# Performance work log

Measured on AMD Instinct MI355X. Metric: run time of the kernel, lower is better.

## Reference

```python
import jax, jax.numpy as jnp
import numpy as np

DIM = 512
HEADS = 8
DIM_HEAD = 64
VID = (8, 32, 32)   # (frames, height, width)
KS = (3, 3, 3)      # odd kernel sizes
DIL = (1, 1, 1)


def _build_indices():
    F, H, W = VID
    kf, kh, kw = KS
    df, dh, dw = DIL
    pf, ph, pw = df * (kf - 1) // 2, dh * (kh - 1) // 2, dw * (kw - 1) // 2
    Fp, Hp, Wp = F + 2 * pf, H + 2 * ph, W + 2 * pw
    N = F * H * W
    ff, yy, xx = np.meshgrid(np.arange(F), np.arange(H), np.arange(W), indexing='ij')
    of, oy, ox = np.meshgrid(np.arange(kf) * df, np.arange(kh) * dh, np.arange(kw) * dw, indexing='ij')
    nf = ff[..., None, None, None] + of   # (F,H,W,kf,kh,kw) coords in padded volume
    ny = yy[..., None, None, None] + oy
    nx = xx[..., None, None, None] + ox
    nbr = ((nf * Hp + ny) * Wp + nx).reshape(N, -1)  # (N, K) flat indices into padded volume
    sf, sy, sx = nf - pf, ny - ph, nx - pw           # source coords in unpadded volume
    valid = (sf >= 0) & (sf < F) & (sy >= 0) & (sy < H) & (sx >= 0) & (sx < W)
    tok = np.where(valid, (sf * H + sy) * W + sx, N).reshape(N, -1)  # sentinel N = padding
    mask = np.arange(N)[:, None] < tok               # causal mask; sentinel N always masked
    mask = np.concatenate([np.zeros((N, 1), bool), mask], axis=1)    # bos column never masked
    return jnp.asarray(nbr), jnp.asarray(mask), ((pf, pf), (ph, ph), (pw, pw))

_NBR, _MASK, _PAD = _build_indices()


def setup_inputs() -> dict:
    key = jax.random.key(0)
    ks = jax.random.split(key, 6)
    F, H, W = VID
    n = F * H * W + 1
    inner = HEADS * DIM_HEAD
    s = DIM ** -0.5
    return {
        "x":     jax.random.normal(ks[0], (1, n, DIM), jnp.float32),
        "w_q":   jax.random.normal(ks[1], (DIM, inner), jnp.float32) * s,
        "w_kv":  jax.random.normal(ks[2], (DIM, 2 * inner), jnp.float32) * s,
        "w_th":  jax.random.normal(ks[3], (HEADS, HEADS), jnp.float32) * HEADS ** -0.5,
        "w_out": jax.random.normal(ks[4], (inner, DIM), jnp.float32) * inner ** -0.5,
        "b_out": jnp.zeros((DIM,), jnp.float32),
    }


def reference(x, w_q, w_kv, w_th, w_out, b_out):
    b, n, _ = x.shape
    F, H, W = VID
    N = F * H * W  # n == N + 1 (BOS token first)
    h, d = HEADS, DIM_HEAD
    q = x @ w_q
    k, v = jnp.split(x @ w_kv, 2, axis=-1)

    def heads(t):
        return t.reshape(b, n, h, d).transpose(0, 2, 1, 3).reshape(b * h, n, d)

    q = heads(q) * d ** -0.5
    k, v = heads(k), heads(v)
    q = q[:, 1:]
    k_bos, k = k[:, :1], k[:, 1:]
    v_bos, v = v[:, :1], v[:, 1:]

    def unfold(t):  # gather 3D local neighborhoods: (bh, N, d) -> (bh, N, K, d)
        vol = jnp.pad(t.reshape(b * h, F, H, W, d), ((0, 0),) + _PAD + ((0, 0),))
        return vol.reshape(b * h, -1, d)[:, _NBR]

    kj = jnp.concatenate([jnp.broadcast_to(k_bos[:, None], (b * h, N, 1, d)), unfold(k)], axis=2)
    vj = jnp.concatenate([jnp.broadcast_to(v_bos[:, None], (b * h, N, 1, d)), unfold(v)], axis=2)

    sim = jnp.einsum('bid,bijd->bij', q, kj)                  # (bh, N, K+1)
    sim = jnp.where(_MASK[None], jnp.finfo(sim.dtype).min, sim)
    attn = jax.nn.softmax(sim, axis=-1)                       # stable_softmax == shift-invariant softmax
    attn = jnp.einsum('gh,bhij->bgij', w_th, attn.reshape(b, h, N, -1)).reshape(b * h, N, -1)
    out = jnp.einsum('bij,bijd->bid', attn, vj)               # (bh, N, d)
    out = jnp.concatenate([v_bos, out], axis=1)               # prepend bos value passthrough
    out = out.reshape(b, h, n, d).transpose(0, 2, 1, 3).reshape(b, n, h * d)
    return out @ w_out + b_out
```

## Files before the change

kernel.cpp:

```cpp
#include <hip/hip_runtime.h>
#include <stdint.h>

#define DIMC 512
#define INNER 512
#define NTOK 8192
#define NSEQ 8193
#define MPAD1 8448
#define QKV_COLS 1536

#define CONV_XT   (MPAD1 * DIMC / 4)
#define CONV_WQKV (QKV_COLS * DIMC)
#define CONV_WOUT (INNER * DIMC)
#define CONV_TOT  (CONV_XT + CONV_WQKV + CONV_WOUT)

typedef __attribute__((ext_vector_type(8))) short bf16x8;
typedef __attribute__((ext_vector_type(4))) float f32x4;
typedef __attribute__((ext_vector_type(8))) unsigned short u16x8;

__device__ __forceinline__ float bf2f(unsigned short u) {
  return __uint_as_float(((unsigned int)u) << 16);
}
__device__ __forceinline__ unsigned short f2bf(float f) {
  unsigned int x = __float_as_uint(f);
  unsigned int lsb = (x >> 16) & 1u;
  x += 0x7fffu + lsb;
  return (unsigned short)(x >> 16);
}

__device__ __forceinline__ void gload_lds16(const unsigned short* g, unsigned short* l) {
  __builtin_amdgcn_global_load_lds(
      (const __attribute__((address_space(1))) void*)g,
      (__attribute__((address_space(3))) void*)l, 16, 0, 0);
}

__global__ void k_conv(const float* __restrict__ x, const float* __restrict__ wq,
                       const float* __restrict__ wkv, const float* __restrict__ wout,
                       unsigned short* __restrict__ xb, unsigned short* __restrict__ wqkvT,
                       unsigned short* __restrict__ woutT) {
  const int gid = blockIdx.x * 256 + threadIdx.x;
  if (gid < CONV_XT) {
    const int idx = gid * 4;
    const int row = idx / DIMC;
    ushort4 o;
    if (row < NSEQ) {
      const float4 v = *(const float4*)(x + idx);
      o.x = f2bf(v.x); o.y = f2bf(v.y); o.z = f2bf(v.z); o.w = f2bf(v.w);
    } else {
      o.x = 0; o.y = 0; o.z = 0; o.w = 0;
    }
    *(ushort4*)(xb + idx) = o;
  } else if (gid < CONV_XT + CONV_WQKV) {
    const int idx = gid - CONV_XT;
    const int c = idx / DIMC, k = idx % DIMC;
    const float v = (c < INNER) ? wq[k * INNER + c] * 0.125f
                                : wkv[k * (2 * INNER) + (c - INNER)];
    wqkvT[idx] = f2bf(v);
  } else {
    const int idx = gid - CONV_XT - CONV_WQKV;
    const int c = idx / DIMC, k = idx % DIMC;
    woutT[idx] = f2bf(wout[k * DIMC + c]);
  }
}

template <int BM, int BN, int TN, int LDC, bool OUT_BF16>
__global__ __launch_bounds__((BM == 256) ? 512 : 256)
void k_gemm(const unsigned short* __restrict__ A,
            const unsigned short* __restrict__ BT,
            void* __restrict__ C,
            const float* __restrict__ bias,
            int Mreal) {
  constexpr int NW = (BM == 256) ? 8 : 4;
  constexpr int MF = (BM == 256) ? 4 : 2;
  constexpr int ISS_A = BM / NW / 8;
  constexpr int ISS_B = BN / NW / 8;
  __shared__ unsigned short As[BM * 64];
  __shared__ unsigned short Bs[BN * 64];

  int flat;
  {
    const int nwg = (int)gridDim.x;
    const int q = nwg >> 3, r = nwg & 7;
    const int xcd = (int)blockIdx.x & 7, idx = (int)blockIdx.x >> 3;
    flat = (xcd < r ? xcd * (q + 1) : r * (q + 1) + (xcd - r) * q) + idx;
  }
  const int tm = flat / TN;
  const int tn = flat % TN;

  const int tid = (int)threadIdx.x;
  const int wave = tid >> 6;
  const int lane = tid & 63;
  int wm, wn;
  if constexpr (BM == 256) { wm = (wave >> 1) * 64; wn = (wave & 1) * 64; }
  else                     { wm = wave * 32;        wn = 0; }

  f32x4 acc[MF][4];
#pragma unroll
  for (int m = 0; m < MF; ++m)
#pragma unroll
    for (int n = 0; n < 4; ++n) {
      acc[m][n][0] = 0.f; acc[m][n][1] = 0.f; acc[m][n][2] = 0.f; acc[m][n][3] = 0.f;
    }

  const size_t a_base = (size_t)tm * BM * DIMC;
  const size_t b_base = (size_t)tn * BN * DIMC;
  const int lrow = lane >> 3;
  const int lk = (lane & 7) * 8;

  for (int k0 = 0; k0 < DIMC; k0 += 64) {
    __syncthreads();
#pragma unroll
    for (int c = 0; c < ISS_A; ++c) {
      const int rA = wave * (BM / NW) + c * 8;
      gload_lds16(A + a_base + (size_t)(rA + lrow) * DIMC + k0 + lk, &As[rA * 64]);
    }
#pragma unroll
    for (int c = 0; c < ISS_B; ++c) {
      const int rB = wave * (BN / NW) + c * 8;
      gload_lds16(BT + b_base + (size_t)(rB + lrow) * DIMC + k0 + lk, &Bs[rB * 64]);
    }
    __syncthreads();

    const int fr = lane & 15;
    const int kg = (lane >> 4) * 8;
#pragma unroll
    for (int kk = 0; kk < 2; ++kk) {
      bf16x8 af[MF], bfr[4];
#pragma unroll
      for (int m = 0; m < MF; ++m)
        af[m] = *(const bf16x8*)&As[(wm + m * 16 + fr) * 64 + kk * 32 + kg];
#pragma unroll
      for (int n = 0; n < 4; ++n)
        bfr[n] = *(const bf16x8*)&Bs[(wn + n * 16 + fr) * 64 + kk * 32 + kg];
#pragma unroll
      for (int m = 0; m < MF; ++m)
#pragma unroll
        for (int n = 0; n < 4; ++n)
          acc[m][n] = __builtin_amdgcn_mfma_f32_16x16x32_bf16(af[m], bfr[n], acc[m][n], 0, 0, 0);
    }
  }

  const int fr = lane & 15;
  const int rg = (lane >> 4) * 4;
#pragma unroll
  for (int m = 0; m < MF; ++m) {
#pragma unroll
    for (int r = 0; r < 4; ++r) {
      const int row = tm * BM + wm + m * 16 + rg + r;
      if (row < Mreal) {
#pragma unroll
        for (int n = 0; n < 4; ++n) {
          const int col = tn * BN + wn + n * 16 + fr;
          const float v = acc[m][n][r];
          if constexpr (OUT_BF16) {
            ((unsigned short*)C)[(size_t)row * LDC + col] = f2bf(v);
          } else {
            ((float*)C)[(size_t)row * LDC + col] = v + bias[col];
          }
        }
      }
    }
  }
}

__global__ __launch_bounds__(256)
void k_attn3(const unsigned short* __restrict__ qkv, const float* __restrict__ w_th,
             unsigned short* __restrict__ Ob) {
  const int bid = (int)blockIdx.x;
  const int t = (int)threadIdx.x;
  if (bid == NTOK / 4) {
    *(unsigned int*)(Ob + 2 * t) = *(const unsigned int*)(qkv + 2 * INNER + 2 * t);
    return;
  }
  const int blk = ((bid & 7) << 8) | (bid >> 3);
  const int w = t >> 6;
  const int l = t & 63;
  const int i = (blk >> 8 << 10) | ((((blk >> 4) & 15) * 2 + (w >> 1)) << 5)
              | ((blk & 15) * 2 + (w & 1));
  const int e = l & 7;
  const int gbase = l & 56;

  int my_pack = -1;
  {
    const int f = i >> 10, rr = i & 1023, y = rr >> 5, xx = rr & 31;
    const int a = l / 9, rem = l % 9, bb = rem / 3, cc = rem % 3;
    const int sf = f + a - 1, sy = y + bb - 1, sx = xx + cc - 1;
    if (l < 27 && (unsigned)sf < 8u && (unsigned)sy < 32u && (unsigned)sx < 32u) {
      const int tk = (sf << 10) | (sy << 5) | sx;
      if (tk <= i) my_pack = tk + 1;
    }
  }
  const unsigned long long mask0 = __ballot(my_pack >= 0);
  const int nval = __popcll(mask0);

  float qf[8];
  {
    const u16x8 q8 = *(const u16x8*)(qkv + (size_t)(i + 1) * QKV_COLS + l * 8);
#pragma unroll
    for (int u = 0; u < 8; ++u) qf[u] = bf2f(q8[u]);
  }

  float s[4] = {-1e30f, -1e30f, -1e30f, -1e30f};
  const unsigned short* kbase = qkv + INNER + l * 8;
  {
    const u16x8 k8 = *(const u16x8*)kbase;
    float p = 0.f;
#pragma unroll
    for (int u = 0; u < 8; ++u) p = fmaf(qf[u], bf2f(k8[u]), p);
    p += __shfl_xor(p, 1); p += __shfl_xor(p, 2); p += __shfl_xor(p, 4);
    if (e == 0) s[0] = p;
  }
  {
    unsigned long long mask = mask0;
    for (int it = 0; it < nval; it += 2) {
      const int l0 = (int)__builtin_ctzll(mask);
      mask &= mask - 1;
      const bool has1 = (it + 1) < nval;
      const int l1 = mask ? (int)__builtin_ctzll(mask) : 0;
      mask &= mask - 1;
      const int pk0 = __shfl(my_pack, l0);
      const int pk1r = __shfl(my_pack, l1);
      const int pk1 = has1 ? pk1r : 0;
      const u16x8 ka = *(const u16x8*)(kbase + (size_t)pk0 * QKV_COLS);
      const u16x8 kb = *(const u16x8*)(kbase + (size_t)pk1 * QKV_COLS);
      float p0 = 0.f, p1 = 0.f;
#pragma unroll
      for (int u = 0; u < 8; ++u) {
        p0 = fmaf(qf[u], bf2f(ka[u]), p0);
        p1 = fmaf(qf[u], bf2f(kb[u]), p1);
      }
      p0 += __shfl_xor(p0, 1); p1 += __shfl_xor(p1, 1);
      p0 += __shfl_xor(p0, 2); p1 += __shfl_xor(p1, 2);
      p0 += __shfl_xor(p0, 4); p1 += __shfl_xor(p1, 4);
      {
        const int js = l0 + 1;
        const bool mine = (e == (js & 7));
        const int pp = js >> 3;
        s[0] = (mine && pp == 0) ? p0 : s[0];
        s[1] = (mine && pp == 1) ? p0 : s[1];
        s[2] = (mine && pp == 2) ? p0 : s[2];
        s[3] = (mine && pp == 3) ? p0 : s[3];
      }
      {
        const int js = l1 + 1;
        const bool mine = has1 && (e == (js & 7));
        const int pp = js >> 3;
        s[0] = (mine && pp == 0) ? p1 : s[0];
        s[1] = (mine && pp == 1) ? p1 : s[1];
        s[2] = (mine && pp == 2) ? p1 : s[2];
        s[3] = (mine && pp == 3) ? p1 : s[3];
      }
    }
  }

  float mx = fmaxf(fmaxf(s[0], s[1]), fmaxf(s[2], s[3]));
  mx = fmaxf(mx, __shfl_xor(mx, 1));
  mx = fmaxf(mx, __shfl_xor(mx, 2));
  mx = fmaxf(mx, __shfl_xor(mx, 4));
  float a4[4]; float sum = 0.f;
#pragma unroll
  for (int p = 0; p < 4; ++p) { a4[p] = __expf(s[p] - mx); sum += a4[p]; }
  sum += __shfl_xor(sum, 1); sum += __shfl_xor(sum, 2); sum += __shfl_xor(sum, 4);
  const float inv = 1.0f / sum;
#pragma unroll
  for (int p = 0; p < 4; ++p) a4[p] *= inv;

  float wth[8];
  {
    const float4 w0 = *(const float4*)(w_th + gbase);
    const float4 w1 = *(const float4*)(w_th + gbase + 4);
    wth[0] = w0.x; wth[1] = w0.y; wth[2] = w0.z; wth[3] = w0.w;
    wth[4] = w1.x; wth[5] = w1.y; wth[6] = w1.z; wth[7] = w1.w;
  }
  float m4[4];
#pragma unroll
  for (int p = 0; p < 4; ++p) {
    float acc = 0.f;
#pragma unroll
    for (int h2 = 0; h2 < 8; ++h2)
      acc = fmaf(wth[h2], __shfl(a4[p], (h2 << 3) | e), acc);
    m4[p] = acc;
  }

  float acc8[8] = {0.f, 0.f, 0.f, 0.f, 0.f, 0.f, 0.f, 0.f};
  float accb[8] = {0.f, 0.f, 0.f, 0.f, 0.f, 0.f, 0.f, 0.f};
  const unsigned short* vbase = qkv + 2 * INNER + l * 8;
  {
    const float mv = __shfl(m4[0], gbase);
    const u16x8 v8 = *(const u16x8*)vbase;
#pragma unroll
    for (int u = 0; u < 8; ++u) acc8[u] = fmaf(mv, bf2f(v8[u]), acc8[u]);
  }
  {
    unsigned long long mask = mask0;
    for (int it = 0; it < nval; it += 2) {
      const int l0 = (int)__builtin_ctzll(mask);
      mask &= mask - 1;
      const bool has1 = (it + 1) < nval;
      const int l1 = mask ? (int)__builtin_ctzll(mask) : 0;
      mask &= mask - 1;
      const int pk0 = __shfl(my_pack, l0);
      const int pk1r = __shfl(my_pack, l1);
      const int pk1 = has1 ? pk1r : 0;
      const u16x8 va = *(const u16x8*)(vbase + (size_t)pk0 * QKV_COLS);
      const u16x8 vb = *(const u16x8*)(vbase + (size_t)pk1 * QKV_COLS);
      const int js0 = l0 + 1;
      const int pp0 = js0 >> 3;
      const float ms0 = pp0 == 0 ? m4[0] : pp0 == 1 ? m4[1] : pp0 == 2 ? m4[2] : m4[3];
      const float mv0 = __shfl(ms0, gbase | (js0 & 7));
      const int js1 = l1 + 1;
      const int pp1 = js1 >> 3;
      const float ms1 = pp1 == 0 ? m4[0] : pp1 == 1 ? m4[1] : pp1 == 2 ? m4[2] : m4[3];
      const float mv1r = __shfl(ms1, gbase | (js1 & 7));
      const float mv1 = has1 ? mv1r : 0.f;
#pragma unroll
      for (int u = 0; u < 8; ++u) {
        acc8[u] = fmaf(mv0, bf2f(va[u]), acc8[u]);
        accb[u] = fmaf(mv1, bf2f(vb[u]), accb[u]);
      }
    }
  }

  u16x8 o;
#pragma unroll
  for (int u = 0; u < 8; ++u) o[u] = f2bf(acc8[u] + accb[u]);
  *(u16x8*)(Ob + (size_t)(i + 1) * INNER + l * 8) = o;
}

extern "C" void kernel_launch(void* const* d_in, const int* in_sizes, int n_in,
                              void* d_out, int out_size, void* d_ws, size_t ws_size,
                              hipStream_t stream) {
  (void)in_sizes; (void)n_in; (void)out_size; (void)ws_size;
  const float* x     = (const float*)d_in[0];
  const float* w_q   = (const float*)d_in[1];
  const float* w_kv  = (const float*)d_in[2];
  const float* w_th  = (const float*)d_in[3];
  const float* w_out = (const float*)d_in[4];
  const float* b_out = (const float*)d_in[5];
  float* out = (float*)d_out;

  char* ws = (char*)d_ws;
  unsigned short* xb    = (unsigned short*)ws;
  unsigned short* wqkvT = (unsigned short*)(ws + 8650752);
  unsigned short* woutT = (unsigned short*)(ws + 10223616);
  unsigned short* qkvb  = (unsigned short*)(ws + 10747904);

  k_conv<<<CONV_TOT / 256, 256, 0, stream>>>(x, w_q, w_kv, w_out, xb, wqkvT, woutT);
  k_gemm<256, 128, QKV_COLS / 128, QKV_COLS, true>
      <<<(MPAD1 / 256) * (QKV_COLS / 128), 512, 0, stream>>>(xb, wqkvT, qkvb, nullptr, NSEQ);
  k_attn3<<<NTOK / 4 + 1, 256, 0, stream>>>(qkvb, w_th, xb);
  k_gemm<128, 64, DIMC / 64, DIMC, false>
      <<<(8320 / 128) * (DIMC / 64), 256, 0, stream>>>(xb, woutT, out, b_out, NSEQ);
}
```

Measured before the change: 70.45 us.

## Double-buffer GEMM LDS tiles and transpose weights via shared-memory tiles

The GEMM kernel now keeps two LDS buffers and issues the global-to-LDS loads for the next K slice while MFMAs run on the current one. This hides load latency and leaves one barrier per iteration instead of two. The QKV GEMM uses a K slice of 32 so that two buffers still fit in LDS. The weight conversion kernel now transposes 64x64 tiles through shared memory, giving coalesced reads and writes in place of strided per-element accesses. One risk: the next stage's global_load_lds writes may race with the current buffer's reads unless a wait on outstanding loads is in place before that buffer is consumed.

```diff
diff --git a/kernel.cpp b/kernel.cpp
--- a/kernel.cpp
+++ b/kernel.cpp
@@ -9,9 +9,9 @@
 #define QKV_COLS 1536
 
 #define CONV_XT   (MPAD1 * DIMC / 4)
-#define CONV_WQKV (QKV_COLS * DIMC)
-#define CONV_WOUT (INNER * DIMC)
-#define CONV_TOT  (CONV_XT + CONV_WQKV + CONV_WOUT)
+#define XBLKS     (CONV_XT / 256)
+#define WQKV_TILES 192
+#define WOUT_TILES 64
 
 typedef __attribute__((ext_vector_type(8))) short bf16x8;
 typedef __attribute__((ext_vector_type(4))) float f32x4;
@@ -37,9 +37,11 @@
                        const float* __restrict__ wkv, const float* __restrict__ wout,
                        unsigned short* __restrict__ xb, unsigned short* __restrict__ wqkvT,
                        unsigned short* __restrict__ woutT) {
-  const int gid = blockIdx.x * 256 + threadIdx.x;
-  if (gid < CONV_XT) {
-    const int idx = gid * 4;
+  __shared__ float tl[64][65];
+  const int bid = (int)blockIdx.x;
+  const int tid = (int)threadIdx.x;
+  if (bid < XBLKS) {
+    const int idx = (bid * 256 + tid) * 4;
     const int row = idx / DIMC;
     ushort4 o;
     if (row < NSEQ) {
@@ -49,20 +51,39 @@
       o.x = 0; o.y = 0; o.z = 0; o.w = 0;
     }
     *(ushort4*)(xb + idx) = o;
-  } else if (gid < CONV_XT + CONV_WQKV) {
-    const int idx = gid - CONV_XT;
-    const int c = idx / DIMC, k = idx % DIMC;
-    const float v = (c < INNER) ? wq[k * INNER + c] * 0.125f
-                                : wkv[k * (2 * INNER) + (c - INNER)];
-    wqkvT[idx] = f2bf(v);
-  } else {
-    const int idx = gid - CONV_XT - CONV_WQKV;
-    const int c = idx / DIMC, k = idx % DIMC;
-    woutT[idx] = f2bf(wout[k * DIMC + c]);
-  }
-}
-
-template <int BM, int BN, int TN, int LDC, bool OUT_BF16>
+    return;
+  }
+  const int tile = bid - XBLKS;
+  const bool is_qkv = tile < WQKV_TILES;
+  const int t2 = is_qkv ? tile : tile - WQKV_TILES;
+  const int k0 = (t2 & 7) * 64;
+  const int c0 = (t2 >> 3) * 64;
+  const int cc = tid & 63;
+  const int rq = tid >> 6;
+#pragma unroll
+  for (int p = 0; p < 16; ++p) {
+    const int r = p * 4 + rq;
+    float v;
+    if (is_qkv) {
+      v = (c0 + cc < INNER) ? wq[(k0 + r) * INNER + c0 + cc] * 0.125f
+                            : wkv[(k0 + r) * (2 * INNER) + c0 + cc - INNER];
+    } else {
+      v = wout[(k0 + r) * DIMC + c0 + cc];
+    }
+    tl[r][cc] = v;
+  }
+  __syncthreads();
+  const int kk = tid & 63;
+#pragma unroll
+  for (int p = 0; p < 16; ++p) {
+    const int c = p * 4 + rq;
+    const unsigned short ov = f2bf(tl[kk][c]);
+    if (is_qkv) wqkvT[(size_t)(c0 + c) * DIMC + k0 + kk] = ov;
+    else        woutT[(size_t)(c0 + c) * DIMC + k0 + kk] = ov;
+  }
+}
+
+template <int BM, int BN, int DBK, int TN, int LDC, bool OUT_BF16>
 __global__ __launch_bounds__((BM == 256) ? 512 : 256)
 void k_gemm(const unsigned short* __restrict__ A,
             const unsigned short* __restrict__ BT,
@@ -71,10 +92,13 @@
             int Mreal) {
   constexpr int NW = (BM == 256) ? 8 : 4;
   constexpr int MF = (BM == 256) ? 4 : 2;
-  constexpr int ISS_A = BM / NW / 8;
-  constexpr int ISS_B = BN / NW / 8;
-  __shared__ unsigned short As[BM * 64];
-  __shared__ unsigned short Bs[BN * 64];
+  constexpr int RPI = 1024 / (DBK * 2);
+  constexpr int ISS_A = (BM / NW) / RPI;
+  constexpr int ISS_B = (BN / NW) / RPI;
+  constexpr int KKN = DBK / 32;
+  constexpr int NT = DIMC / DBK;
+  __shared__ unsigned short As[2][BM * DBK];
+  __shared__ unsigned short Bs[2][BN * DBK];
 
   int flat;
   {
@@ -103,43 +127,48 @@
 
   const size_t a_base = (size_t)tm * BM * DIMC;
   const size_t b_base = (size_t)tn * BN * DIMC;
-  const int lrow = lane >> 3;
-  const int lk = (lane & 7) * 8;
-
-  for (int k0 = 0; k0 < DIMC; k0 += 64) {
-    __syncthreads();
+  const int lrow = lane / (DBK / 8);
+  const int lk = (lane % (DBK / 8)) * 8;
+
+  auto stage = [&](int buf, int k0) {
 #pragma unroll
     for (int c = 0; c < ISS_A; ++c) {
-      const int rA = wave * (BM / NW) + c * 8;
-      gload_lds16(A + a_base + (size_t)(rA + lrow) * DIMC + k0 + lk, &As[rA * 64]);
+      const int rA = wave * (BM / NW) + c * RPI;
+      gload_lds16(A + a_base + (size_t)(rA + lrow) * DIMC + k0 + lk, &As[buf][rA * DBK]);
     }
 #pragma unroll
     for (int c = 0; c < ISS_B; ++c) {
-      const int rB = wave * (BN / NW) + c * 8;
-      gload_lds16(BT + b_base + (size_t)(rB + lrow) * DIMC + k0 + lk, &Bs[rB * 64]);
-    }
-    __syncthreads();
-
-    const int fr = lane & 15;
-    const int kg = (lane >> 4) * 8;
-#pragma unroll
-    for (int kk = 0; kk < 2; ++kk) {
+      const int rB = wave * (BN / NW) + c * RPI;
+      gload_lds16(BT + b_base + (size_t)(rB + lrow) * DIMC + k0 + lk, &Bs[buf][rB * DBK]);
+    }
+  };
+
+  stage(0, 0);
+  __syncthreads();
+
+  const int fr = lane & 15;
+  const int kg = (lane >> 4) * 8;
+  for (int t = 0; t < NT; ++t) {
+    const int cur = t & 1;
+    if (t + 1 < NT) stage(cur ^ 1, (t + 1) * DBK);
+#pragma unroll
+    for (int kk = 0; kk < KKN; ++kk) {
       bf16x8 af[MF], bfr[4];
 #pragma unroll
       for (int m = 0; m < MF; ++m)
-        af[m] = *(const bf16x8*)&As[(wm + m * 16 + fr) * 64 + kk * 32 + kg];
+        af[m] = *(const bf16x8*)&As[cur][(wm + m * 16 + fr) * DBK + kk * 32 + kg];
 #pragma unroll
       for (int n = 0; n < 4; ++n)
-        bfr[n] = *(const bf16x8*)&Bs[(wn + n * 16 + fr) * 64 + kk * 32 + kg];
+        bfr[n] = *(const bf16x8*)&Bs[cur][(wn + n * 16 + fr) * DBK + kk * 32 + kg];
 #pragma unroll
       for (int m = 0; m < MF; ++m)
 #pragma unroll
         for (int n = 0; n < 4; ++n)
           acc[m][n] = __builtin_amdgcn_mfma_f32_16x16x32_bf16(af[m], bfr[n], acc[m][n], 0, 0, 0);
     }
-  }
-
-  const int fr = lane & 15;
+    __syncthreads();
+  }
+
   const int rg = (lane >> 4) * 4;
 #pragma unroll
   for (int m = 0; m < MF; ++m) {
@@ -344,10 +373,11 @@
   unsigned short* woutT = (unsigned short*)(ws + 10223616);
   unsigned short* qkvb  = (unsigned short*)(ws + 10747904);
 
-  k_conv<<<CONV_TOT / 256, 256, 0, stream>>>(x, w_q, w_kv, w_out, xb, wqkvT, woutT);
-  k_gemm<256, 128, QKV_COLS / 128, QKV_COLS, true>
+  k_conv<<<XBLKS + WQKV_TILES + WOUT_TILES, 256, 0, stream>>>(
+      x, w_q, w_kv, w_out, xb, wqkvT, woutT);
+  k_gemm<256, 128, 32, QKV_COLS / 128, QKV_COLS, true>
       <<<(MPAD1 / 256) * (QKV_COLS / 128), 512, 0, stream>>>(xb, wqkvT, qkvb, nullptr, NSEQ);
   k_attn3<<<NTOK / 4 + 1, 256, 0, stream>>>(qkvb, w_th, xb);
-  k_gemm<128, 64, DIMC / 64, DIMC, false>
+  k_gemm<128, 64, 64, DIMC / 64, DIMC, false>
       <<<(8320 / 128) * (DIMC / 64), 256, 0, stream>>>(xb, woutT, out, b_out, NSEQ);
 }
```

Measured after the change: 71.75 us. Within noise of the previous version (+1.8%).

## Stage shared K/V neighborhoods in LDS for 2x2x2 query blocks; tile weight transpose

Applied to the files above, without the earlier changes.

The attention kernel now handles a 2x2x2 block of query tokens per 512-thread workgroup. It loads the shared 4x4x4 K halo, and later the V halo, into LDS with global_load_lds, so the eight queries reuse neighbour rows instead of each doing its own scattered global reads. The weight conversion kernel now transposes through a padded 64x64 shared tile so that both reads and writes are coalesced. The cost is 64KB of LDS per block and extra barriers, which limits occupancy, and each block loads halo rows that may be masked out.

```diff
diff --git a/kernel.cpp b/kernel.cpp
--- a/kernel.cpp
+++ b/kernel.cpp
@@ -8,10 +8,9 @@
 #define MPAD1 8448
 #define QKV_COLS 1536
 
-#define CONV_XT   (MPAD1 * DIMC / 4)
-#define CONV_WQKV (QKV_COLS * DIMC)
-#define CONV_WOUT (INNER * DIMC)
-#define CONV_TOT  (CONV_XT + CONV_WQKV + CONV_WOUT)
+#define WTILES 256
+#define CONV_XT (MPAD1 * DIMC / 4)
+#define XBLKS   (CONV_XT / 256)
 
 typedef __attribute__((ext_vector_type(8))) short bf16x8;
 typedef __attribute__((ext_vector_type(4))) float f32x4;
@@ -37,9 +36,11 @@
                        const float* __restrict__ wkv, const float* __restrict__ wout,
                        unsigned short* __restrict__ xb, unsigned short* __restrict__ wqkvT,
                        unsigned short* __restrict__ woutT) {
-  const int gid = blockIdx.x * 256 + threadIdx.x;
-  if (gid < CONV_XT) {
-    const int idx = gid * 4;
+  __shared__ float tl[64][65];
+  const int bid = (int)blockIdx.x;
+  const int tid = (int)threadIdx.x;
+  if (bid >= WTILES) {
+    const int idx = ((bid - WTILES) * 256 + tid) * 4;
     const int row = idx / DIMC;
     ushort4 o;
     if (row < NSEQ) {
@@ -49,16 +50,34 @@
       o.x = 0; o.y = 0; o.z = 0; o.w = 0;
     }
     *(ushort4*)(xb + idx) = o;
-  } else if (gid < CONV_XT + CONV_WQKV) {
-    const int idx = gid - CONV_XT;
-    const int c = idx / DIMC, k = idx % DIMC;
-    const float v = (c < INNER) ? wq[k * INNER + c] * 0.125f
-                                : wkv[k * (2 * INNER) + (c - INNER)];
-    wqkvT[idx] = f2bf(v);
-  } else {
-    const int idx = gid - CONV_XT - CONV_WQKV;
-    const int c = idx / DIMC, k = idx % DIMC;
-    woutT[idx] = f2bf(wout[k * DIMC + c]);
+    return;
+  }
+  const bool is_qkv = bid < 192;
+  const int t2 = is_qkv ? bid : bid - 192;
+  const int k0 = (t2 & 7) * 64;
+  const int c0 = (t2 >> 3) * 64;
+  const int cc = tid & 63;
+  const int rq = tid >> 6;
+#pragma unroll
+  for (int p = 0; p < 16; ++p) {
+    const int r = p * 4 + rq;
+    float v;
+    if (is_qkv) {
+      v = (c0 + cc < INNER) ? wq[(k0 + r) * INNER + c0 + cc] * 0.125f
+                            : wkv[(k0 + r) * (2 * INNER) + c0 + cc - INNER];
+    } else {
+      v = wout[(k0 + r) * DIMC + c0 + cc];
+    }
+    tl[r][cc] = v;
+  }
+  __syncthreads();
+  const int kk = tid & 63;
+#pragma unroll
+  for (int p = 0; p < 16; ++p) {
+    const int c = p * 4 + rq;
+    const unsigned short ov = f2bf(tl[kk][c]);
+    if (is_qkv) wqkvT[(size_t)(c0 + c) * DIMC + k0 + kk] = ov;
+    else        woutT[(size_t)(c0 + c) * DIMC + k0 + kk] = ov;
   }
 }
 
@@ -162,31 +181,43 @@
   }
 }
 
-__global__ __launch_bounds__(256)
-void k_attn3(const unsigned short* __restrict__ qkv, const float* __restrict__ w_th,
+__global__ __launch_bounds__(512)
+void k_attn4(const unsigned short* __restrict__ qkv, const float* __restrict__ w_th,
              unsigned short* __restrict__ Ob) {
+  __shared__ unsigned short tile[64 * 512];
   const int bid = (int)blockIdx.x;
   const int t = (int)threadIdx.x;
-  if (bid == NTOK / 4) {
-    *(unsigned int*)(Ob + 2 * t) = *(const unsigned int*)(qkv + 2 * INNER + 2 * t);
+  if (bid == NTOK / 8) {
+    if (t < INNER) Ob[t] = qkv[2 * INNER + t];
     return;
   }
-  const int blk = ((bid & 7) << 8) | (bid >> 3);
+  const int blk = ((bid & 7) << 7) | (bid >> 3);
   const int w = t >> 6;
   const int l = t & 63;
-  const int i = (blk >> 8 << 10) | ((((blk >> 4) & 15) * 2 + (w >> 1)) << 5)
-              | ((blk & 15) * 2 + (w & 1));
+  const int f0 = (blk >> 8) * 2, y0 = ((blk >> 4) & 15) * 2, x0 = (blk & 15) * 2;
+  const int df = w >> 2, dy = (w >> 1) & 1, dx = w & 1;
+  const int fi = f0 + df, yi = y0 + dy, xi = x0 + dx;
+  const int i = (fi << 10) | (yi << 5) | xi;
   const int e = l & 7;
   const int gbase = l & 56;
 
+#pragma unroll
+  for (int is = 0; is < 8; ++is) {
+    const int s = is * 8 + w;
+    const int sf = f0 - 1 + (s >> 4), sy = y0 - 1 + ((s >> 2) & 3), sx = x0 - 1 + (s & 3);
+    int row = 0;
+    if ((unsigned)sf < 8u && (unsigned)sy < 32u && (unsigned)sx < 32u)
+      row = ((sf << 10) | (sy << 5) | sx) + 1;
+    gload_lds16(qkv + (size_t)row * QKV_COLS + INNER + l * 8, &tile[s * 512]);
+  }
+
   int my_pack = -1;
   {
-    const int f = i >> 10, rr = i & 1023, y = rr >> 5, xx = rr & 31;
-    const int a = l / 9, rem = l % 9, bb = rem / 3, cc = rem % 3;
-    const int sf = f + a - 1, sy = y + bb - 1, sx = xx + cc - 1;
+    const int a = l / 9, rem = l % 9, b = rem / 3, c = rem % 3;
+    const int sf = fi + a - 1, sy = yi + b - 1, sx = xi + c - 1;
     if (l < 27 && (unsigned)sf < 8u && (unsigned)sy < 32u && (unsigned)sx < 32u) {
       const int tk = (sf << 10) | (sy << 5) | sx;
-      if (tk <= i) my_pack = tk + 1;
+      if (tk <= i) my_pack = (df + a) * 16 + (dy + b) * 4 + (dx + c);
     }
   }
   const unsigned long long mask0 = __ballot(my_pack >= 0);
@@ -198,17 +229,19 @@
 #pragma unroll
     for (int u = 0; u < 8; ++u) qf[u] = bf2f(q8[u]);
   }
-
-  float s[4] = {-1e30f, -1e30f, -1e30f, -1e30f};
-  const unsigned short* kbase = qkv + INNER + l * 8;
-  {
-    const u16x8 k8 = *(const u16x8*)kbase;
+  float sbos;
+  {
+    const u16x8 k8 = *(const u16x8*)(qkv + INNER + l * 8);
     float p = 0.f;
 #pragma unroll
     for (int u = 0; u < 8; ++u) p = fmaf(qf[u], bf2f(k8[u]), p);
     p += __shfl_xor(p, 1); p += __shfl_xor(p, 2); p += __shfl_xor(p, 4);
-    if (e == 0) s[0] = p;
-  }
+    sbos = p;
+  }
+  __syncthreads();
+
+  float s[4] = {-1e30f, -1e30f, -1e30f, -1e30f};
+  if (e == 0) s[0] = sbos;
   {
     unsigned long long mask = mask0;
     for (int it = 0; it < nval; it += 2) {
@@ -217,11 +250,11 @@
       const bool has1 = (it + 1) < nval;
       const int l1 = mask ? (int)__builtin_ctzll(mask) : 0;
       mask &= mask - 1;
-      const int pk0 = __shfl(my_pack, l0);
-      const int pk1r = __shfl(my_pack, l1);
-      const int pk1 = has1 ? pk1r : 0;
-      const u16x8 ka = *(const u16x8*)(kbase + (size_t)pk0 * QKV_COLS);
-      const u16x8 kb = *(const u16x8*)(kbase + (size_t)pk1 * QKV_COLS);
+      const int sl0 = __shfl(my_pack, l0);
+      const int sl1r = __shfl(my_pack, l1);
+      const int sl1 = (has1 && sl1r >= 0) ? sl1r : 0;
+      const u16x8 ka = *(const u16x8*)&tile[sl0 * 512 + l * 8];
+      const u16x8 kb = *(const u16x8*)&tile[sl1 * 512 + l * 8];
       float p0 = 0.f, p1 = 0.f;
 #pragma unroll
       for (int u = 0; u < 8; ++u) {
@@ -251,6 +284,17 @@
       }
     }
   }
+  __syncthreads();
+
+#pragma unroll
+  for (int is = 0; is < 8; ++is) {
+    const int s = is * 8 + w;
+    const int sf = f0 - 1 + (s >> 4), sy = y0 - 1 + ((s >> 2) & 3), sx = x0 - 1 + (s & 3);
+    int row = 0;
+    if ((unsigned)sf < 8u && (unsigned)sy < 32u && (unsigned)sx < 32u)
+      row = ((sf << 10) | (sy << 5) | sx) + 1;
+    gload_lds16(qkv + (size_t)row * QKV_COLS + 2 * INNER + l * 8, &tile[s * 512]);
+  }
 
   float mx = fmaxf(fmaxf(s[0], s[1]), fmaxf(s[2], s[3]));
   mx = fmaxf(mx, __shfl_xor(mx, 1));
@@ -283,13 +327,14 @@
 
   float acc8[8] = {0.f, 0.f, 0.f, 0.f, 0.f, 0.f, 0.f, 0.f};
   float accb[8] = {0.f, 0.f, 0.f, 0.f, 0.f, 0.f, 0.f, 0.f};
-  const unsigned short* vbase = qkv + 2 * INNER + l * 8;
   {
     const float mv = __shfl(m4[0], gbase);
-    const u16x8 v8 = *(const u16x8*)vbase;
+    const u16x8 v8 = *(const u16x8*)(qkv + 2 * INNER + l * 8);
 #pragma unroll
     for (int u = 0; u < 8; ++u) acc8[u] = fmaf(mv, bf2f(v8[u]), acc8[u]);
   }
+  __syncthreads();
+
   {
     unsigned long long mask = mask0;
     for (int it = 0; it < nval; it += 2) {
@@ -298,11 +343,11 @@
       const bool has1 = (it + 1) < nval;
       const int l1 = mask ? (int)__builtin_ctzll(mask) : 0;
       mask &= mask - 1;
-      const int pk0 = __shfl(my_pack, l0);
-      const int pk1r = __shfl(my_pack, l1);
-      const int pk1 = has1 ? pk1r : 0;
-      const u16x8 va = *(const u16x8*)(vbase + (size_t)pk0 * QKV_COLS);
-      const u16x8 vb = *(const u16x8*)(vbase + (size_t)pk1 * QKV_COLS);
+      const int sl0 = __shfl(my_pack, l0);
+      const int sl1r = __shfl(my_pack, l1);
+      const int sl1 = (has1 && sl1r >= 0) ? sl1r : 0;
+      const u16x8 va = *(const u16x8*)&tile[sl0 * 512 + l * 8];
+      const u16x8 vb = *(const u16x8*)&tile[sl1 * 512 + l * 8];
       const int js0 = l0 + 1;
       const int pp0 = js0 >> 3;
       const float ms0 = pp0 == 0 ? m4[0] : pp0 == 1 ? m4[1] : pp0 == 2 ? m4[2] : m4[3];
@@ -344,10 +389,10 @@
   unsigned short* woutT = (unsigned short*)(ws + 10223616);
   unsigned short* qkvb  = (unsigned short*)(ws + 10747904);
 
-  k_conv<<<CONV_TOT / 256, 256, 0, stream>>>(x, w_q, w_kv, w_out, xb, wqkvT, woutT);
+  k_conv<<<WTILES + XBLKS, 256, 0, stream>>>(x, w_q, w_kv, w_out, xb, wqkvT, woutT);
   k_gemm<256, 128, QKV_COLS / 128, QKV_COLS, true>
       <<<(MPAD1 / 256) * (QKV_COLS / 128), 512, 0, stream>>>(xb, wqkvT, qkvb, nullptr, NSEQ);
-  k_attn3<<<NTOK / 4 + 1, 256, 0, stream>>>(qkvb, w_th, xb);
+  k_attn4<<<NTOK / 8 + 1, 512, 0, stream>>>(qkvb, w_th, xb);
   k_gemm<128, 64, DIMC / 64, DIMC, false>
       <<<(8320 / 128) * (DIMC / 64), 256, 0, stream>>>(xb, woutT, out, b_out, NSEQ);
 }
```

New measurement: 77.23 us. 1.1x slower.
